# Performance work log

Hardware: AMD Instinct MI355X
Metric: run time of the kernel (lower is better)

## Reference

```python
import jax, jax.numpy as jnp
import numpy as np

NUM_EXPERTS = 64
TOP_K = 2
CAP_FACTOR = 1.0


def setup_inputs() -> dict:
    key = jax.random.key(0)
    k1, k2 = jax.random.split(key)
    x = jax.random.normal(k1, (8192, 4096), dtype=jnp.float32)
    wg = jax.random.normal(k2, (NUM_EXPERTS, 4096), dtype=jnp.float32) * 0.02
    return {"x": x, "wg": wg}


def reference(x, wg):
    # x: [S, M] tokens, wg: [E, M] gate weight (Linear, no bias)
    S, M = x.shape
    E, K = NUM_EXPERTS, TOP_K
    capacity = K * int(CAP_FACTOR * ((S + E - 1) // E))  # static

    logits = jnp.einsum('sm,em->se', x, wg)            # [S, E]
    gates = jax.nn.softmax(logits, axis=1)             # [S, E]
    _, topk_idx = jax.lax.top_k(logits, K)             # [S, K]

    masks = jax.nn.one_hot(topk_idx, E, dtype=x.dtype)  # [S, K, E]
    gates_s = jnp.einsum('se,ske->sk', gates, masks)    # [S, K]

    # load-balancing loss (fp32 path of load_balance)
    me = jnp.sum(gates, axis=0)                         # [E]
    ce = jnp.sum(masks[:, 0], axis=0)                   # [E]
    l_loss = jnp.sum(me * ce) * (E / (S * S))

    # capacity locations: cumsum-sub-one per k, offset by counts of earlier k's
    locs = jnp.cumsum(masks, axis=0) - 1.0              # [S, K, E]
    counts = jnp.sum(masks, axis=0)                     # [K, E]
    acc = jnp.concatenate([jnp.zeros((1, E), x.dtype),
                           jnp.cumsum(counts, axis=0)[:-1]], axis=0)  # [K, E]
    locs = locs + acc[None, :, :]
    loc_s = jnp.einsum('ske,ske->sk', locs, masks).astype(jnp.int32)  # [S, K]

    # postnorm gate normalization (top_k > 1)
    eps = jnp.finfo(gates_s.dtype).eps
    gates_n = gates_s / jnp.clip(jnp.sum(gates_s, axis=1, keepdims=True), eps)

    idx = topk_idx.astype(jnp.int32)                    # [S, K]
    valid = (loc_s >= 0) & (loc_s < capacity)           # [S, K]
    pos = jnp.where(valid, idx * capacity + loc_s, 0)   # [S, K] flat slot ids

    # encode: scatter tokens (unweighted, is_postnorm=True) into [E*capacity, M]
    contrib = jnp.where(valid[..., None], x[:, None, :], 0.0)  # [S, K, M]
    dispatched = jnp.zeros((E * capacity, M), x.dtype)
    dispatched = dispatched.at[pos.reshape(-1)].add(contrib.reshape(-1, M))

    # expert_fn = identity (world_size=1, routing pipeline is the op under test)
    expert_output = dispatched                          # [E*capacity, M]

    # decode: gather back and combine with normalized gates
    gathered = expert_output[pos.reshape(-1)].reshape(S, K, M)
    out = jnp.einsum('sk,skm->sm', gates_n * valid.astype(x.dtype), gathered)
    return out, l_loss
```

## Files before the change

### kernel.cpp

```cpp
#include <hip/hip_runtime.h>
#include <math.h>

#define S_TOK 8192
#define M_DIM 4096
#define NEXP 64
#define CAPACITY 256
#define NCHUNK 128

__global__ __launch_bounds__(256) void k_gate(
    const float* __restrict__ x, const float* __restrict__ wg,
    float* __restrict__ me_g, int* __restrict__ idx0_g, int* __restrict__ idx1_g,
    float* __restrict__ gn0_g, float* __restrict__ gn1_g)
{
    constexpr int BT = 32, BK = 64;
    __shared__ __align__(16) float xs[2][BK][BT + 1];
    __shared__ __align__(16) float wsl[2][BK][NEXP + 4];
    __shared__ float lgs[BT][NEXP + 1];
    __shared__ float me_sh[NEXP];

    const int tid = threadIdx.x;
    const int t0 = blockIdx.x * BT;
    if (tid < NEXP) me_sh[tid] = 0.f;

    const int tx = tid & 15;
    const int ty = tid >> 4;
    float acc[2][4] = {{0.f,0.f,0.f,0.f},{0.f,0.f,0.f,0.f}};

    float4 rx[2], rw[4];
    const float* xb = x + (size_t)t0 * M_DIM;

    auto ldchunk = [&](int kc) {
        #pragma unroll
        for (int i = 0; i < 2; ++i) {
            int item = tid + 256 * i, tok = item >> 4, kq = item & 15;
            rx[i] = *(const float4*)(xb + (size_t)tok * M_DIM + kc + 4 * kq);
        }
        #pragma unroll
        for (int i = 0; i < 4; ++i) {
            int item = tid + 256 * i, e = item >> 4, kq = item & 15;
            rw[i] = *(const float4*)(wg + (size_t)e * M_DIM + kc + 4 * kq);
        }
    };
    auto stchunk = [&](int buf) {
        #pragma unroll
        for (int i = 0; i < 2; ++i) {
            int item = tid + 256 * i, tok = item >> 4, kq = item & 15;
            xs[buf][4*kq+0][tok] = rx[i].x;
            xs[buf][4*kq+1][tok] = rx[i].y;
            xs[buf][4*kq+2][tok] = rx[i].z;
            xs[buf][4*kq+3][tok] = rx[i].w;
        }
        #pragma unroll
        for (int i = 0; i < 4; ++i) {
            int item = tid + 256 * i, e = item >> 4, kq = item & 15;
            wsl[buf][4*kq+0][e] = rw[i].x;
            wsl[buf][4*kq+1][e] = rw[i].y;
            wsl[buf][4*kq+2][e] = rw[i].z;
            wsl[buf][4*kq+3][e] = rw[i].w;
        }
    };

    ldchunk(0);
    stchunk(0);
    __syncthreads();
    const int NC = M_DIM / BK;
    for (int c = 0; c < NC; ++c) {
        const int buf = c & 1;
        if (c + 1 < NC) ldchunk((c + 1) * BK);
        #pragma unroll 16
        for (int kk = 0; kk < BK; ++kk) {
            float a0 = xs[buf][kk][2*ty];
            float a1 = xs[buf][kk][2*ty + 1];
            const float4 b = *(const float4*)&wsl[buf][kk][4*tx];
            acc[0][0] = fmaf(a0, b.x, acc[0][0]);
            acc[0][1] = fmaf(a0, b.y, acc[0][1]);
            acc[0][2] = fmaf(a0, b.z, acc[0][2]);
            acc[0][3] = fmaf(a0, b.w, acc[0][3]);
            acc[1][0] = fmaf(a1, b.x, acc[1][0]);
            acc[1][1] = fmaf(a1, b.y, acc[1][1]);
            acc[1][2] = fmaf(a1, b.z, acc[1][2]);
            acc[1][3] = fmaf(a1, b.w, acc[1][3]);
        }
        __syncthreads();
        if (c + 1 < NC) stchunk(buf ^ 1);
        __syncthreads();
    }

    #pragma unroll
    for (int i = 0; i < 2; ++i)
        #pragma unroll
        for (int j = 0; j < 4; ++j)
            lgs[2*ty + i][4*tx + j] = acc[i][j];
    __syncthreads();

    const int wv = tid >> 6, lane = tid & 63;
    float me_acc = 0.f;
    for (int i = 0; i < 8; ++i) {
        const int t = wv * 8 + i;
        const float lg = lgs[t][lane];

        float v = lg; int id = lane;
        #pragma unroll
        for (int off = 32; off > 0; off >>= 1) {
            float v2 = __shfl_xor(v, off);
            int   i2 = __shfl_xor(id, off);
            if (v2 > v || (v2 == v && i2 < id)) { v = v2; id = i2; }
        }
        const float mx = v; const int i0 = id;

        const float p = expf(lg - mx);
        float sum = p;
        #pragma unroll
        for (int off = 32; off > 0; off >>= 1) sum += __shfl_xor(sum, off);
        me_acc += p / sum;

        float v1 = (lane == i0) ? -INFINITY : lg; int id1 = lane;
        #pragma unroll
        for (int off = 32; off > 0; off >>= 1) {
            float v2 = __shfl_xor(v1, off);
            int   i2 = __shfl_xor(id1, off);
            if (v2 > v1 || (v2 == v1 && i2 < id1)) { v1 = v2; id1 = i2; }
        }

        const float g0 = 1.0f / sum;
        const float g1 = expf(v1 - mx) / sum;
        const float den = fmaxf(g0 + g1, 1.1920929e-07f);
        if (lane == 0) {
            const int gs = t0 + t;
            idx0_g[gs] = i0;
            idx1_g[gs] = id1;
            gn0_g[gs] = g0 / den;
            gn1_g[gs] = g1 / den;
        }
    }
    atomicAdd(&me_sh[lane], me_acc);
    __syncthreads();
    if (tid < NEXP) atomicAdd(&me_g[tid], me_sh[tid]);
}

__global__ __launch_bounds__(64) void k_rank(
    const int* __restrict__ idx0_g, const int* __restrict__ idx1_g,
    int* __restrict__ rank0_g, int* __restrict__ rank1_g,
    int* __restrict__ cnt_g )
{
    const int lane = threadIdx.x;
    const int chunk = blockIdx.x;
    const int s = chunk * 64 + lane;
    const int e0 = idx0_g[s], e1 = idx1_g[s];
    const unsigned long long lt = (1ull << lane) - 1ull;

    int r0 = 0, r1 = 0, c0 = 0, c1 = 0;
    #pragma unroll
    for (int e = 0; e < 64; ++e) {
        unsigned long long m0 = __ballot(e0 == e);
        unsigned long long m1 = __ballot(e1 == e);
        if (e0 == e) r0 = __popcll(m0 & lt);
        if (e1 == e) r1 = __popcll(m1 & lt);
        if (lane == e) { c0 = __popcll(m0); c1 = __popcll(m1); }
    }
    rank0_g[s] = r0;
    rank1_g[s] = r1;
    cnt_g[chunk * 64 + lane] = c0;
    cnt_g[NCHUNK * 64 + chunk * 64 + lane] = c1;
}

__global__ __launch_bounds__(128) void k_scan(
    const int* __restrict__ cnt_g, int* __restrict__ base_g,
    int* __restrict__ tot0_g, const float* __restrict__ me_g,
    float* __restrict__ loss_out)
{
    __shared__ float red[NEXP];
    const int tid = threadIdx.x;
    const int k = tid >> 6, e = tid & 63;
    const int* cnt = cnt_g + k * NCHUNK * 64 + e;
    int* base = base_g + k * NCHUNK * 64 + e;
    int run = 0;
    #pragma unroll 8
    for (int c = 0; c < NCHUNK; ++c) {
        base[c * 64] = run;
        run += cnt[c * 64];
    }
    if (k == 0) {
        tot0_g[e] = run;
        red[e] = me_g[e] * (float)run;
    }
    __syncthreads();
    if (tid == 0) {
        float t = 0.f;
        for (int i = 0; i < NEXP; ++i) t += red[i];
        *loss_out = t * (float)(64.0 / (8192.0 * 8192.0));
    }
}

__global__ __launch_bounds__(256) void k_out(
    const float* __restrict__ x, float* __restrict__ out,
    const int* __restrict__ idx0_g, const int* __restrict__ idx1_g,
    const float* __restrict__ gn0_g, const float* __restrict__ gn1_g,
    const int* __restrict__ rank0_g, const int* __restrict__ rank1_g,
    const int* __restrict__ base_g, const int* __restrict__ tot0_g)
{
    __shared__ float wsh;
    const int s = blockIdx.x;
    const int tid = threadIdx.x;
    if (tid == 0) {
        const int chunk = s >> 6;
        const int e0 = idx0_g[s], e1 = idx1_g[s];
        const int loc0 = base_g[chunk * 64 + e0] + rank0_g[s];
        const int loc1 = base_g[NCHUNK * 64 + chunk * 64 + e1] + rank1_g[s] + tot0_g[e1];
        float w = 0.f;
        if (loc0 < CAPACITY) w += gn0_g[s];
        if (loc1 < CAPACITY) w += gn1_g[s];
        wsh = w;
    }
    __syncthreads();
    const float w = wsh;
    const float4* xr = (const float4*)(x + (size_t)s * M_DIM);
    float4* orow = (float4*)(out + (size_t)s * M_DIM);
    #pragma unroll
    for (int i = 0; i < 4; ++i) {
        float4 v = xr[tid + 256 * i];
        v.x *= w; v.y *= w; v.z *= w; v.w *= w;
        orow[tid + 256 * i] = v;
    }
}

extern "C" void kernel_launch(void* const* d_in, const int* in_sizes, int n_in,
                              void* d_out, int out_size, void* d_ws, size_t ws_size,
                              hipStream_t stream)
{
    const float* x  = (const float*)d_in[0];
    const float* wg = (const float*)d_in[1];
    float* out = (float*)d_out;

    float* me   = (float*)d_ws;
    int*  idx0  = (int*)d_ws + 64;
    int*  idx1  = idx0 + S_TOK;
    float* gn0  = (float*)(idx1 + S_TOK);
    float* gn1  = gn0 + S_TOK;
    int*  rank0 = (int*)(gn1 + S_TOK);
    int*  rank1 = rank0 + S_TOK;
    int*  cnt   = rank1 + S_TOK;
    int*  base  = cnt + 2 * NCHUNK * 64;
    int*  tot0  = base + 2 * NCHUNK * 64;

    hipMemsetAsync(me, 0, NEXP * sizeof(float), stream);
    k_gate<<<S_TOK / 32, 256, 0, stream>>>(x, wg, me, idx0, idx1, gn0, gn1);
    k_rank<<<NCHUNK, 64, 0, stream>>>(idx0, idx1, rank0, rank1, cnt);
    k_scan<<<1, 128, 0, stream>>>(cnt, base, tot0, me,
                                  out + (size_t)S_TOK * M_DIM);
    k_out<<<S_TOK, 256, 0, stream>>>(x, out, idx0, idx1, gn0, gn1,
                                     rank0, rank1, base, tot0);
}
```

Measured before the change: 355.5 us.

## Split-K gate GEMM with separate reduce, parallel scan, and precomputed token weights

The gate logits GEMM now splits K eight ways into 1024 blocks of 64 tokens with 4x4 register tiles and XOR-swizzled shared memory, writing partial sums that a new reduce kernel adds up before softmax and top-2. The single-block serial scan becomes a wave-parallel shuffle scan over 32 blocks, with the loss accumulated by atomics. Per-token combine weights move into a small kernel, so the output kernel only reads one weight per row. The aim is more parallelism and less serial latency in the gating and scan stages, at the cost of extra launches and partial-sum traffic through global memory.

```diff
diff --git a/kernel.cpp b/kernel.cpp
--- a/kernel.cpp
+++ b/kernel.cpp
@@ -6,98 +6,106 @@
 #define NEXP 64
 #define CAPACITY 256
 #define NCHUNK 128
-
-__global__ __launch_bounds__(256) void k_gate(
+#define KS 8
+#define KSL 512
+#define BT 64
+#define BK 32
+#define NC (KSL / BK)
+
+__global__ __launch_bounds__(256) void k_logits(
     const float* __restrict__ x, const float* __restrict__ wg,
-    float* __restrict__ me_g, int* __restrict__ idx0_g, int* __restrict__ idx1_g,
-    float* __restrict__ gn0_g, float* __restrict__ gn1_g)
-{
-    constexpr int BT = 32, BK = 64;
-    __shared__ __align__(16) float xs[2][BK][BT + 1];
-    __shared__ __align__(16) float wsl[2][BK][NEXP + 4];
-    __shared__ float lgs[BT][NEXP + 1];
-    __shared__ float me_sh[NEXP];
-
+    float* __restrict__ part)
+{
+    __shared__ float xs[2][BK * 64];
+    __shared__ float wsl[2][BK * 64];
     const int tid = threadIdx.x;
-    const int t0 = blockIdx.x * BT;
-    if (tid < NEXP) me_sh[tid] = 0.f;
+    const int tile = blockIdx.x >> 3;
+    const int ks   = blockIdx.x & 7;
+    const int t0 = tile * BT;
+    const int kb = ks * KSL;
 
     const int tx = tid & 15;
     const int ty = tid >> 4;
-    float acc[2][4] = {{0.f,0.f,0.f,0.f},{0.f,0.f,0.f,0.f}};
-
-    float4 rx[2], rw[4];
-    const float* xb = x + (size_t)t0 * M_DIM;
-
-    auto ldchunk = [&](int kc) {
+
+    float4 rx[2], rw[2];
+    auto ld = [&](int kc) {
         #pragma unroll
         for (int i = 0; i < 2; ++i) {
-            int item = tid + 256 * i, tok = item >> 4, kq = item & 15;
-            rx[i] = *(const float4*)(xb + (size_t)tok * M_DIM + kc + 4 * kq);
-        }
-        #pragma unroll
-        for (int i = 0; i < 4; ++i) {
-            int item = tid + 256 * i, e = item >> 4, kq = item & 15;
-            rw[i] = *(const float4*)(wg + (size_t)e * M_DIM + kc + 4 * kq);
+            const int item = tid + 256 * i;
+            const int r = item >> 3, kq = item & 7;
+            rx[i] = *(const float4*)(x  + (size_t)(t0 + r) * M_DIM + kc + 4 * kq);
+            rw[i] = *(const float4*)(wg + (size_t)r       * M_DIM + kc + 4 * kq);
         }
     };
-    auto stchunk = [&](int buf) {
+    auto st = [&](int buf) {
         #pragma unroll
         for (int i = 0; i < 2; ++i) {
-            int item = tid + 256 * i, tok = item >> 4, kq = item & 15;
-            xs[buf][4*kq+0][tok] = rx[i].x;
-            xs[buf][4*kq+1][tok] = rx[i].y;
-            xs[buf][4*kq+2][tok] = rx[i].z;
-            xs[buf][4*kq+3][tok] = rx[i].w;
-        }
-        #pragma unroll
-        for (int i = 0; i < 4; ++i) {
-            int item = tid + 256 * i, e = item >> 4, kq = item & 15;
-            wsl[buf][4*kq+0][e] = rw[i].x;
-            wsl[buf][4*kq+1][e] = rw[i].y;
-            wsl[buf][4*kq+2][e] = rw[i].z;
-            wsl[buf][4*kq+3][e] = rw[i].w;
+            const int item = tid + 256 * i;
+            const int r = item >> 3, kq = item & 7;
+            const int quad = r >> 2, lo = r & 3;
+            const float vx[4] = {rx[i].x, rx[i].y, rx[i].z, rx[i].w};
+            const float vw[4] = {rw[i].x, rw[i].y, rw[i].z, rw[i].w};
+            #pragma unroll
+            for (int j = 0; j < 4; ++j) {
+                const int row = 4 * kq + j;
+                const int addr = row * 64 + ((quad ^ kq) << 2) + lo;
+                xs[buf][addr]  = vx[j];
+                wsl[buf][addr] = vw[j];
+            }
         }
     };
 
-    ldchunk(0);
-    stchunk(0);
+    float acc[4][4] = {};
+    ld(kb);
+    st(0);
     __syncthreads();
-    const int NC = M_DIM / BK;
     for (int c = 0; c < NC; ++c) {
         const int buf = c & 1;
-        if (c + 1 < NC) ldchunk((c + 1) * BK);
-        #pragma unroll 16
+        if (c + 1 < NC) ld(kb + (c + 1) * BK);
+        #pragma unroll 8
         for (int kk = 0; kk < BK; ++kk) {
-            float a0 = xs[buf][kk][2*ty];
-            float a1 = xs[buf][kk][2*ty + 1];
-            const float4 b = *(const float4*)&wsl[buf][kk][4*tx];
-            acc[0][0] = fmaf(a0, b.x, acc[0][0]);
-            acc[0][1] = fmaf(a0, b.y, acc[0][1]);
-            acc[0][2] = fmaf(a0, b.z, acc[0][2]);
-            acc[0][3] = fmaf(a0, b.w, acc[0][3]);
-            acc[1][0] = fmaf(a1, b.x, acc[1][0]);
-            acc[1][1] = fmaf(a1, b.y, acc[1][1]);
-            acc[1][2] = fmaf(a1, b.z, acc[1][2]);
-            acc[1][3] = fmaf(a1, b.w, acc[1][3]);
+            const int sw = kk >> 2;
+            const float4 a = *(const float4*)&xs [buf][kk * 64 + ((ty ^ sw) << 2)];
+            const float4 b = *(const float4*)&wsl[buf][kk * 64 + ((tx ^ sw) << 2)];
+            const float av[4] = {a.x, a.y, a.z, a.w};
+            const float bv[4] = {b.x, b.y, b.z, b.w};
+            #pragma unroll
+            for (int i = 0; i < 4; ++i)
+                #pragma unroll
+                for (int j = 0; j < 4; ++j)
+                    acc[i][j] = fmaf(av[i], bv[j], acc[i][j]);
         }
         __syncthreads();
-        if (c + 1 < NC) stchunk(buf ^ 1);
+        if (c + 1 < NC) st(buf ^ 1);
         __syncthreads();
     }
 
     #pragma unroll
-    for (int i = 0; i < 2; ++i)
-        #pragma unroll
-        for (int j = 0; j < 4; ++j)
-            lgs[2*ty + i][4*tx + j] = acc[i][j];
+    for (int i = 0; i < 4; ++i) {
+        float4 v;
+        v.x = acc[i][0]; v.y = acc[i][1]; v.z = acc[i][2]; v.w = acc[i][3];
+        *(float4*)(part + ((size_t)ks * S_TOK + t0 + 4 * ty + i) * NEXP + 4 * tx) = v;
+    }
+}
+
+__global__ __launch_bounds__(256) void k_reduce(
+    const float* __restrict__ part, float* __restrict__ me_g,
+    int* __restrict__ idx0_g, int* __restrict__ idx1_g,
+    float* __restrict__ gn0_g, float* __restrict__ gn1_g)
+{
+    __shared__ float me_sh[NEXP];
+    const int tid = threadIdx.x;
+    if (tid < NEXP) me_sh[tid] = 0.f;
     __syncthreads();
 
     const int wv = tid >> 6, lane = tid & 63;
     float me_acc = 0.f;
     for (int i = 0; i < 8; ++i) {
-        const int t = wv * 8 + i;
-        const float lg = lgs[t][lane];
+        const int t = blockIdx.x * 32 + wv * 8 + i;
+        float lg = 0.f;
+        #pragma unroll
+        for (int s = 0; s < KS; ++s)
+            lg += part[((size_t)s * S_TOK + t) * NEXP + lane];
 
         float v = lg; int id = lane;
         #pragma unroll
@@ -126,11 +134,10 @@
         const float g1 = expf(v1 - mx) / sum;
         const float den = fmaxf(g0 + g1, 1.1920929e-07f);
         if (lane == 0) {
-            const int gs = t0 + t;
-            idx0_g[gs] = i0;
-            idx1_g[gs] = id1;
-            gn0_g[gs] = g0 / den;
-            gn1_g[gs] = g1 / den;
+            idx0_g[t] = i0;
+            idx1_g[t] = id1;
+            gn0_g[t] = g0 / den;
+            gn1_g[t] = g1 / den;
         }
     }
     atomicAdd(&me_sh[lane], me_acc);
@@ -164,63 +171,65 @@
     cnt_g[NCHUNK * 64 + chunk * 64 + lane] = c1;
 }
 
-__global__ __launch_bounds__(128) void k_scan(
+__global__ __launch_bounds__(256) void k_scan(
     const int* __restrict__ cnt_g, int* __restrict__ base_g,
     int* __restrict__ tot0_g, const float* __restrict__ me_g,
     float* __restrict__ loss_out)
 {
-    __shared__ float red[NEXP];
-    const int tid = threadIdx.x;
-    const int k = tid >> 6, e = tid & 63;
-    const int* cnt = cnt_g + k * NCHUNK * 64 + e;
-    int* base = base_g + k * NCHUNK * 64 + e;
-    int run = 0;
-    #pragma unroll 8
-    for (int c = 0; c < NCHUNK; ++c) {
-        base[c * 64] = run;
-        run += cnt[c * 64];
-    }
-    if (k == 0) {
-        tot0_g[e] = run;
-        red[e] = me_g[e] * (float)run;
-    }
-    __syncthreads();
-    if (tid == 0) {
-        float t = 0.f;
-        for (int i = 0; i < NEXP; ++i) t += red[i];
-        *loss_out = t * (float)(64.0 / (8192.0 * 8192.0));
-    }
-}
-
-__global__ __launch_bounds__(256) void k_out(
-    const float* __restrict__ x, float* __restrict__ out,
+    const int wv = threadIdx.x >> 6, lane = threadIdx.x & 63;
+    const int g = blockIdx.x * 4 + wv;
+    const int k = g >> 6, e = g & 63;
+
+    const int c0 = cnt_g[(k * NCHUNK + 2 * lane)     * 64 + e];
+    const int c1 = cnt_g[(k * NCHUNK + 2 * lane + 1) * 64 + e];
+    const int s = c0 + c1;
+    int incl = s;
+    #pragma unroll
+    for (int d = 1; d < 64; d <<= 1) {
+        int v = __shfl_up(incl, d);
+        if (lane >= d) incl += v;
+    }
+    const int excl = incl - s;
+    base_g[(k * NCHUNK + 2 * lane)     * 64 + e] = excl;
+    base_g[(k * NCHUNK + 2 * lane + 1) * 64 + e] = excl + c0;
+    const int total = __shfl(incl, 63);
+    if (k == 0 && lane == 0) {
+        tot0_g[e] = total;
+        atomicAdd(loss_out, me_g[e] * (float)total * 9.5367431640625e-07f);
+    }
+}
+
+__global__ __launch_bounds__(256) void k_weight(
     const int* __restrict__ idx0_g, const int* __restrict__ idx1_g,
     const float* __restrict__ gn0_g, const float* __restrict__ gn1_g,
     const int* __restrict__ rank0_g, const int* __restrict__ rank1_g,
-    const int* __restrict__ base_g, const int* __restrict__ tot0_g)
-{
-    __shared__ float wsh;
+    const int* __restrict__ base_g, const int* __restrict__ tot0_g,
+    float* __restrict__ w_g)
+{
+    const int s = blockIdx.x * 256 + threadIdx.x;
+    const int chunk = s >> 6;
+    const int e0 = idx0_g[s], e1 = idx1_g[s];
+    const int loc0 = base_g[chunk * 64 + e0] + rank0_g[s];
+    const int loc1 = base_g[(NCHUNK + chunk) * 64 + e1] + rank1_g[s] + tot0_g[e1];
+    float w = 0.f;
+    if (loc0 < CAPACITY) w += gn0_g[s];
+    if (loc1 < CAPACITY) w += gn1_g[s];
+    w_g[s] = w;
+}
+
+__global__ __launch_bounds__(256) void k_out(
+    const float* __restrict__ x, const float* __restrict__ w_g,
+    float* __restrict__ out)
+{
     const int s = blockIdx.x;
-    const int tid = threadIdx.x;
-    if (tid == 0) {
-        const int chunk = s >> 6;
-        const int e0 = idx0_g[s], e1 = idx1_g[s];
-        const int loc0 = base_g[chunk * 64 + e0] + rank0_g[s];
-        const int loc1 = base_g[NCHUNK * 64 + chunk * 64 + e1] + rank1_g[s] + tot0_g[e1];
-        float w = 0.f;
-        if (loc0 < CAPACITY) w += gn0_g[s];
-        if (loc1 < CAPACITY) w += gn1_g[s];
-        wsh = w;
-    }
-    __syncthreads();
-    const float w = wsh;
+    const float w = w_g[s];
     const float4* xr = (const float4*)(x + (size_t)s * M_DIM);
-    float4* orow = (float4*)(out + (size_t)s * M_DIM);
+    float4* o = (float4*)(out + (size_t)s * M_DIM);
     #pragma unroll
     for (int i = 0; i < 4; ++i) {
-        float4 v = xr[tid + 256 * i];
+        float4 v = xr[threadIdx.x + 256 * i];
         v.x *= w; v.y *= w; v.z *= w; v.w *= w;
-        orow[tid + 256 * i] = v;
+        o[threadIdx.x + 256 * i] = v;
     }
 }
 
@@ -231,9 +240,11 @@
     const float* x  = (const float*)d_in[0];
     const float* wg = (const float*)d_in[1];
     float* out = (float*)d_out;
-
-    float* me   = (float*)d_ws;
-    int*  idx0  = (int*)d_ws + 64;
+    float* loss = out + (size_t)S_TOK * M_DIM;
+
+    float* part = (float*)d_ws;
+    float* me   = part + (size_t)KS * S_TOK * NEXP;
+    int*  idx0  = (int*)(me + NEXP);
     int*  idx1  = idx0 + S_TOK;
     float* gn0  = (float*)(idx1 + S_TOK);
     float* gn1  = gn0 + S_TOK;
@@ -242,12 +253,16 @@
     int*  cnt   = rank1 + S_TOK;
     int*  base  = cnt + 2 * NCHUNK * 64;
     int*  tot0  = base + 2 * NCHUNK * 64;
+    float* wtok = (float*)(tot0 + NEXP);
 
     hipMemsetAsync(me, 0, NEXP * sizeof(float), stream);
-    k_gate<<<S_TOK / 32, 256, 0, stream>>>(x, wg, me, idx0, idx1, gn0, gn1);
+    hipMemsetAsync(loss, 0, sizeof(float), stream);
+
+    k_logits<<<128 * KS, 256, 0, stream>>>(x, wg, part);
+    k_reduce<<<S_TOK / 32, 256, 0, stream>>>(part, me, idx0, idx1, gn0, gn1);
     k_rank<<<NCHUNK, 64, 0, stream>>>(idx0, idx1, rank0, rank1, cnt);
-    k_scan<<<1, 128, 0, stream>>>(cnt, base, tot0, me,
-                                  out + (size_t)S_TOK * M_DIM);
-    k_out<<<S_TOK, 256, 0, stream>>>(x, out, idx0, idx1, gn0, gn1,
-                                     rank0, rank1, base, tot0);
-}
+    k_scan<<<32, 256, 0, stream>>>(cnt, base, tot0, me, loss);
+    k_weight<<<S_TOK / 256, 256, 0, stream>>>(idx0, idx1, gn0, gn1,
+                                              rank0, rank1, base, tot0, wtok);
+    k_out<<<S_TOK, 256, 0, stream>>>(x, wtok, out);
+}
```

Result: faster. 310.8 us (-12.6%).
